# Kernel tuning notes

Hardware: AMD Instinct MI355X
Metric: run time of the kernel (lower is better)

## Reference

```python
import jax, jax.numpy as jnp
import numpy as np

EMBED = 1024
HEADS = 16
HEAD_DIM = EMBED // HEADS
SCALE = HEAD_DIM ** -0.5


def setup_inputs() -> dict:
    key = jax.random.key(0)
    ks = jax.random.split(key, 11)
    B, S, D = 2, 2048, EMBED
    s = D ** -0.5
    return {
        "Q": jax.random.normal(ks[0], (B, S, D), jnp.float32),
        "K": jax.random.normal(ks[1], (B, S, D), jnp.float32),
        "V": jax.random.normal(ks[2], (B, S, D), jnp.float32),
        "Wq": jax.random.normal(ks[3], (D, D), jnp.float32) * s,
        "bq": jax.random.normal(ks[4], (D,), jnp.float32) * 0.01,
        "Wk": jax.random.normal(ks[5], (D, D), jnp.float32) * s,
        "bk": jax.random.normal(ks[6], (D,), jnp.float32) * 0.01,
        "Wv": jax.random.normal(ks[7], (D, D), jnp.float32) * s,
        "bv": jax.random.normal(ks[8], (D,), jnp.float32) * 0.01,
        "Wo": jax.random.normal(ks[9], (D, D), jnp.float32) * s,
        "bo": jax.random.normal(ks[10], (D,), jnp.float32) * 0.01,
    }


def reference(Q, K, V, Wq, bq, Wk, bk, Wv, bv, Wo, bo):
    N, S, D = Q.shape
    H, Hd = HEADS, HEAD_DIM
    # linear projections (x @ W + b), then split heads: [N, S, H, Hd]
    q = (Q @ Wq + bq).reshape(N, S, H, Hd)
    k = (K @ Wk + bk).reshape(N, S, H, Hd)
    v = (V @ Wv + bv).reshape(N, S, H, Hd)
    # scaled dot-product attention, full [N,H,S,S] scores as in the original
    energy = jnp.einsum('nqhd,nkhd->nhqk', q, k) * SCALE
    attn = jax.nn.softmax(energy, axis=3)
    out = jnp.einsum('nhql,nlhd->nqhd', attn, v).reshape(N, S, D)
    return out @ Wo + bo
```

## Files before the change

### kernel.cpp

```cpp
#include <hip/hip_runtime.h>
#include <cstdint>


typedef _Float16 h8 __attribute__((ext_vector_type(8)));
typedef float f4 __attribute__((ext_vector_type(4)));
typedef float f16v __attribute__((ext_vector_type(16)));
typedef unsigned int u32x4 __attribute__((ext_vector_type(4)));
typedef const unsigned int __attribute__((address_space(1)))* gp1_t;
typedef unsigned int __attribute__((address_space(3)))* lp3_t;

#define FSWZ(r) ((((r) ^ ((r) >> 3))) & 7)

__device__ __forceinline__ void gld_lds16(const void* g, const void* l) {
  __builtin_amdgcn_global_load_lds((gp1_t)(uintptr_t)g,
                                   (lp3_t)(unsigned int)(uintptr_t)l, 16, 0, 0);
}
__device__ __forceinline__ unsigned pkh(float a, float b) {
  return __builtin_bit_cast(unsigned, __builtin_amdgcn_cvt_pkrtz(a, b));
}
__device__ __forceinline__ void plswap(unsigned& a, unsigned& b) {
  asm volatile("v_permlane32_swap_b32 %0, %1" : "+v"(a), "+v"(b));
}


__global__ void cvt_w4(const float* __restrict__ wq, const float* __restrict__ wk,
                       const float* __restrict__ wv, const float* __restrict__ wo,
                       _Float16* __restrict__ WT) {
  const int z = blockIdx.z;
  const float* W = (z == 0) ? wq : (z == 1) ? wk : (z == 2) ? wv : wo;
  _Float16* o = WT + (size_t)z * 1048576;
  const int k = blockIdx.x * 256 + threadIdx.x;
  const int n0 = blockIdx.y * 4;
  float4 w = *(const float4*)(W + (size_t)k * 1024 + n0);
  o[(size_t)(n0 + 0) * 1024 + k] = (_Float16)w.x;
  o[(size_t)(n0 + 1) * 1024 + k] = (_Float16)w.y;
  o[(size_t)(n0 + 2) * 1024 + k] = (_Float16)w.z;
  o[(size_t)(n0 + 3) * 1024 + k] = (_Float16)w.w;
}


#define A_LOAD(KT)                                                             \
  do {                                                                         \
    _Pragma("unroll") for (int i_ = 0; i_ < 4; ++i_) {                         \
      const int idx_ = i_ * 256 + tid;                                         \
      const int r_ = idx_ >> 3, g_ = idx_ & 7;                                 \
      const float* ap_ = A32 + (size_t)(row0 + r_) * 1024 + (KT) * 64 + g_ * 8;\
      fa[i_] = *(const float4*)ap_;                                            \
      fb[i_] = *(const float4*)(ap_ + 4);                                      \
    }                                                                          \
  } while (0)

#define A_WRITE(BUF)                                                           \
  do {                                                                         \
    _Pragma("unroll") for (int i_ = 0; i_ < 4; ++i_) {                         \
      const int idx_ = i_ * 256 + tid;                                         \
      const int r_ = idx_ >> 3, g_ = idx_ & 7;                                 \
      u32x4 w_ = {pkh(fa[i_].x, fa[i_].y), pkh(fa[i_].z, fa[i_].w),            \
                  pkh(fb[i_].x, fb[i_].y), pkh(fb[i_].z, fb[i_].w)};           \
      *(u32x4*)&As[BUF][r_ * 64 + ((g_ ^ FSWZ(r_)) << 3)] = w_;                \
    }                                                                          \
  } while (0)

#define B_STAGE(BUF, KT)                                                       \
  do {                                                                         \
    _Pragma("unroll") for (int rr_ = 0; rr_ < 4; ++rr_) {                      \
      const int idx_ = rr_ * 256 + tid;                                        \
      const int r_ = idx_ >> 3, g_ = idx_ & 7;                                 \
      gld_lds16(Bt + (size_t)(col0 + r_) * 1024 + (KT) * 64 + (g_ ^ FSWZ(r_)) * 8,\
                &Bs[BUF][(rr_ * 256 + wave * 64) * 8]);                        \
    }                                                                          \
  } while (0)

__global__ __launch_bounds__(256, 2) void gemm_qkv(const float* __restrict__ Qf,
                                                   const float* __restrict__ Kf,
                                                   const float* __restrict__ Vf,
                                                   const _Float16* __restrict__ WT,
                                                   const float* __restrict__ bq,
                                                   const float* __restrict__ bk,
                                                   const float* __restrict__ bv,
                                                   _Float16* __restrict__ qkv16) {
  __shared__ _Float16 As[2][8192];
  __shared__ _Float16 Bs[2][8192];
  const int z = blockIdx.z;
  const float* A32 = (z == 0) ? Qf : (z == 1) ? Kf : Vf;
  const _Float16* Bt = WT + (size_t)z * 1048576;
  const float* bias = (z == 0) ? bq : (z == 1) ? bk : bv;
  _Float16* out16 = qkv16 + (size_t)z * 4194304;
  const int tid = threadIdx.x;
  const int wave = tid >> 6, lane = tid & 63;
  const int lg = lane >> 4, ll = lane & 15;
  const int wr = wave >> 1, wc = wave & 1;
  const int row0 = blockIdx.x * 128, col0 = blockIdx.y * 128;
  f4 acc[4][4] = {};
  float4 fa[4], fb[4];
  A_LOAD(0);
  B_STAGE(0, 0);
  A_WRITE(0);
  __syncthreads();
  int cur = 0;
  for (int kt = 0; kt < 16; ++kt) {
    const bool pre = (kt + 1 < 16);
    if (pre) { A_LOAD(kt + 1); B_STAGE(cur ^ 1, kt + 1); }
#pragma unroll
    for (int kk = 0; kk < 2; ++kk) {
      h8 af[4], bf[4];
#pragma unroll
      for (int mi = 0; mi < 4; ++mi) {
        const int r = wr * 64 + mi * 16 + ll;
        af[mi] = *(const h8*)&As[cur][r * 64 + (((kk * 4 + lg) ^ FSWZ(r)) << 3)];
      }
#pragma unroll
      for (int ni = 0; ni < 4; ++ni) {
        const int r = wc * 64 + ni * 16 + ll;
        bf[ni] = *(const h8*)&Bs[cur][r * 64 + (((kk * 4 + lg) ^ FSWZ(r)) << 3)];
      }
#pragma unroll
      for (int mi = 0; mi < 4; ++mi)
#pragma unroll
        for (int ni = 0; ni < 4; ++ni)
          acc[mi][ni] = __builtin_amdgcn_mfma_f32_16x16x32_f16(af[mi], bf[ni],
                                                               acc[mi][ni], 0, 0, 0);
    }
    if (pre) A_WRITE(cur ^ 1);
    __syncthreads();
    cur ^= 1;
  }
#pragma unroll
  for (int ni = 0; ni < 4; ++ni) {
    const int c = col0 + wc * 64 + ni * 16 + ll;
    const float bv = bias[c];
#pragma unroll
    for (int mi = 0; mi < 4; ++mi) {
#pragma unroll
      for (int i = 0; i < 4; ++i) {
        const int r = row0 + wr * 64 + mi * 16 + lg * 4 + i;
        const float val = acc[mi][ni][i] + bv;
        const int b = r >> 11, s = r & 2047, h = c >> 6, hd = c & 63;
        out16[((size_t)((b * 16 + h) * 2048 + s)) * 64 + hd] = (_Float16)val;
      }
    }
  }
}


#define G_STAGE16(BUF, KT)                                                     \
  do {                                                                         \
    _Pragma("unroll") for (int rr_ = 0; rr_ < 4; ++rr_) {                      \
      const int idx_ = rr_ * 256 + tid;                                        \
      const int r_ = idx_ >> 3, g_ = idx_ & 7;                                 \
      const int lb_ = (rr_ * 256 + wave * 64) * 8;                             \
      gld_lds16(A16 + (size_t)(row0 + r_) * 1024 + (KT) * 64 + (g_ ^ FSWZ(r_)) * 8,\
                &As[BUF][lb_]);                                                \
      gld_lds16(WoT + (size_t)(col0 + r_) * 1024 + (KT) * 64 + (g_ ^ FSWZ(r_)) * 8,\
                &Bs[BUF][lb_]);                                                \
    }                                                                          \
  } while (0)

__global__ __launch_bounds__(256, 2) void gemm_out_k(const _Float16* __restrict__ A16,
                                                     const _Float16* __restrict__ WoT,
                                                     const float* __restrict__ bo,
                                                     float* __restrict__ out) {
  __shared__ _Float16 As[2][8192];
  __shared__ _Float16 Bs[2][8192];
  const int tid = threadIdx.x;
  const int wave = tid >> 6, lane = tid & 63;
  const int lg = lane >> 4, ll = lane & 15;
  const int wr = wave >> 1, wc = wave & 1;
  const int row0 = blockIdx.x * 128, col0 = blockIdx.y * 128;
  f4 acc[4][4] = {};
  G_STAGE16(0, 0);
  __syncthreads();
  int cur = 0;
  for (int kt = 0; kt < 16; ++kt) {
    if (kt + 1 < 16) G_STAGE16(cur ^ 1, kt + 1);
#pragma unroll
    for (int kk = 0; kk < 2; ++kk) {
      h8 af[4], bf[4];
#pragma unroll
      for (int mi = 0; mi < 4; ++mi) {
        const int r = wr * 64 + mi * 16 + ll;
        af[mi] = *(const h8*)&As[cur][r * 64 + (((kk * 4 + lg) ^ FSWZ(r)) << 3)];
      }
#pragma unroll
      for (int ni = 0; ni < 4; ++ni) {
        const int r = wc * 64 + ni * 16 + ll;
        bf[ni] = *(const h8*)&Bs[cur][r * 64 + (((kk * 4 + lg) ^ FSWZ(r)) << 3)];
      }
#pragma unroll
      for (int mi = 0; mi < 4; ++mi)
#pragma unroll
        for (int ni = 0; ni < 4; ++ni)
          acc[mi][ni] = __builtin_amdgcn_mfma_f32_16x16x32_f16(af[mi], bf[ni],
                                                               acc[mi][ni], 0, 0, 0);
    }
    __syncthreads();
    cur ^= 1;
  }
#pragma unroll
  for (int ni = 0; ni < 4; ++ni) {
    const int c = col0 + wc * 64 + ni * 16 + ll;
    const float bv = bo[c];
#pragma unroll
    for (int mi = 0; mi < 4; ++mi)
#pragma unroll
      for (int i = 0; i < 4; ++i) {
        const int r = row0 + wr * 64 + mi * 16 + lg * 4 + i;
        out[(size_t)r * 1024 + c] = acc[mi][ni][i] + bv;
      }
  }
}


#define STAGE_K(BUF, KT)                                                      \
  do {                                                                        \
    _Pragma("unroll") for (int rr_ = 0; rr_ < 2; ++rr_) {                     \
      const int idx_ = rr_ * 256 + tid;                                       \
      const int r_ = idx_ >> 3, g_ = idx_ & 7;                                \
      gld_lds16(kbp + (size_t)((KT) * 64 + r_) * 64 + ((g_ ^ FSWZ(r_)) * 8),  \
                &Ks[BUF][(rr_ * 256 + wave * 64) * 8]);                       \
    }                                                                         \
  } while (0)

#define LOAD_V(KT, VA, VC)                                                    \
  do {                                                                        \
    const _Float16* vp_ = vbp + (size_t)((KT) * 64 + vkey0) * 64 + vhd0;      \
    VA = *(const uint4*)vp_;                                                  \
    VC = *(const uint4*)(vp_ + 64);                                           \
  } while (0)

#define WRITE_V(BUF, VA, VC)                                                  \
  do {                                                                        \
    const unsigned short* pa_ = (const unsigned short*)&VA;                   \
    const unsigned short* pc_ = (const unsigned short*)&VC;                   \
    _Pragma("unroll") for (int j_ = 0; j_ < 8; ++j_) {                        \
      const int row_ = vhd0 + j_;                                             \
      *(unsigned*)&Vt[BUF][row_ * 64 + (((vkey0 >> 3) ^ FSWZ(row_)) << 3) +   \
                           (vkey0 & 7)] =                                     \
          (unsigned)pa_[j_] | ((unsigned)pc_[j_] << 16);                      \
    }                                                                         \
  } while (0)

#define PV_STEP(SX, PP, KBP)                                                  \
  do {                                                                        \
    unsigned wA = pkh(SX[(PP) + 0], SX[(PP) + 1]);                            \
    unsigned wB = pkh(SX[(PP) + 2], SX[(PP) + 3]);                            \
    unsigned wC = pkh(SX[(PP) + 4], SX[(PP) + 5]);                            \
    unsigned wD = pkh(SX[(PP) + 6], SX[(PP) + 7]);                            \
    plswap(wA, wC);                                                           \
    plswap(wB, wD);                                                           \
    u32x4 afu = {wA, wB, wC, wD};                                             \
    h8 af = __builtin_bit_cast(h8, afu);                                      \
    const int c_ = (KBP) * 2 + hi;                                            \
    h8 vf0 = *(const h8*)&Vt[cur][l31 * 64 + ((c_ ^ FSWZ(l31)) << 3)];        \
    h8 vf1 = *(const h8*)&Vt[cur][(32 + l31) * 64 +                           \
                                  ((c_ ^ FSWZ(32 + l31)) << 3)];              \
    acc0 = __builtin_amdgcn_mfma_f32_32x32x16_f16(af, vf0, acc0, 0, 0, 0);    \
    acc1 = __builtin_amdgcn_mfma_f32_32x32x16_f16(af, vf1, acc1, 0, 0, 0);    \
  } while (0)

__global__ __launch_bounds__(256, 4) void attn_kernel(
    const _Float16* __restrict__ q16, const _Float16* __restrict__ k16,
    const _Float16* __restrict__ v16, _Float16* __restrict__ Op,
    float2* __restrict__ mlp) {
  __shared__ _Float16 Ks[2][4096];
  __shared__ _Float16 Vt[2][4096];
  __shared__ float Fb[4][32];
  const int tid = threadIdx.x;
  const int wave = tid >> 6, lane = tid & 63;
  const int l31 = lane & 31, hi = lane >> 5;
  const int blk = blockIdx.x;
  const int xcd = blk & 7, j = blk >> 3;
  const int bh = xcd * 4 + (j >> 5);
  const int split = (j >> 4) & 1;
  const int qb = j & 15;
  const int q0w = qb * 128 + wave * 32;
  const _Float16* qbp = q16 + (size_t)bh * 131072;
  const _Float16* kbp = k16 + (size_t)bh * 131072 + (size_t)split * 65536;
  const _Float16* vbp = v16 + (size_t)bh * 131072 + (size_t)split * 65536;
  const int vkey0 = (tid & 31) * 2, vhd0 = (tid >> 5) * 8;

  h8 qf0 = *(const h8*)(qbp + (size_t)(q0w + l31) * 64 + 0 + hi * 8);
  h8 qf1 = *(const h8*)(qbp + (size_t)(q0w + l31) * 64 + 16 + hi * 8);
  h8 qf2 = *(const h8*)(qbp + (size_t)(q0w + l31) * 64 + 32 + hi * 8);
  h8 qf3 = *(const h8*)(qbp + (size_t)(q0w + l31) * 64 + 48 + hi * 8);

  f16v acc0 = {}, acc1 = {};
  float mval = -1e30f, lsum = 0.f;
  const float C = 0.125f * 1.44269504089f;

  uint4 va, vc;
  STAGE_K(0, 0);
  LOAD_V(0, va, vc);
  WRITE_V(0, va, vc);
  __syncthreads();

  int cur = 0;
  for (int kt = 0; kt < 16; ++kt) {
    const bool pre = (kt + 1 < 16);
    if (pre) { STAGE_K(cur ^ 1, kt + 1); LOAD_V(kt + 1, va, vc); }

    f16v s0 = {}, s1 = {};
    __builtin_amdgcn_s_setprio(1);
#pragma unroll
    for (int kc = 0; kc < 4; ++kc) {
      const int c = kc * 2 + hi;
      h8 k0 = *(const h8*)&Ks[cur][l31 * 64 + ((c ^ FSWZ(l31)) << 3)];
      h8 k1 = *(const h8*)&Ks[cur][(32 + l31) * 64 + ((c ^ FSWZ(32 + l31)) << 3)];
      h8 qf = (kc == 0) ? qf0 : (kc == 1) ? qf1 : (kc == 2) ? qf2 : qf3;
      s0 = __builtin_amdgcn_mfma_f32_32x32x16_f16(k0, qf, s0, 0, 0, 0);
      s1 = __builtin_amdgcn_mfma_f32_32x32x16_f16(k1, qf, s1, 0, 0, 0);
    }
    __builtin_amdgcn_s_setprio(0);

    float t[8];
#pragma unroll
    for (int j2 = 0; j2 < 8; ++j2)
      t[j2] = fmaxf(fmaxf(s0[j2], s0[j2 + 8]), fmaxf(s1[j2], s1[j2 + 8]));
    float pm = fmaxf(fmaxf(fmaxf(t[0], t[1]), fmaxf(t[2], t[3])),
                     fmaxf(fmaxf(t[4], t[5]), fmaxf(t[6], t[7])));
    pm = fmaxf(pm, __shfl_xor(pm, 32));
    const float pms = pm * C;

    if (__any(pms > mval + 8.0f)) {
      const float mnew = fmaxf(mval, pms);
      const float f = __builtin_amdgcn_exp2f(mval - mnew);
      mval = mnew;
      lsum *= f;
      Fb[wave][l31] = f;
      const f4 fr0 = *(const f4*)&Fb[wave][0 + 4 * hi];
      const f4 fr1 = *(const f4*)&Fb[wave][8 + 4 * hi];
      const f4 fr2 = *(const f4*)&Fb[wave][16 + 4 * hi];
      const f4 fr3 = *(const f4*)&Fb[wave][24 + 4 * hi];
#pragma unroll
      for (int r = 0; r < 16; ++r) {
        const float fx = (r < 4 ? fr0 : r < 8 ? fr1 : r < 12 ? fr2 : fr3)[r & 3];
        acc0[r] *= fx;
        acc1[r] *= fx;
      }
    }

#pragma unroll
    for (int r = 0; r < 16; ++r) {
      s0[r] = __builtin_amdgcn_exp2f(s0[r] * C - mval);
      s1[r] = __builtin_amdgcn_exp2f(s1[r] * C - mval);
    }
    float z[8];
#pragma unroll
    for (int j2 = 0; j2 < 8; ++j2)
      z[j2] = (s0[j2] + s0[j2 + 8]) + (s1[j2] + s1[j2 + 8]);
    lsum += ((z[0] + z[1]) + (z[2] + z[3])) + ((z[4] + z[5]) + (z[6] + z[7]));

    __builtin_amdgcn_s_setprio(1);
    PV_STEP(s0, 0, 0);
    PV_STEP(s0, 8, 1);
    PV_STEP(s1, 0, 2);
    PV_STEP(s1, 8, 3);
    __builtin_amdgcn_s_setprio(0);

    if (pre) WRITE_V(cur ^ 1, va, vc);
    __syncthreads();
    cur ^= 1;
  }

  lsum += __shfl_xor(lsum, 32);
  if (!hi) mlp[split * 65536 + bh * 2048 + q0w + l31] = make_float2(mval, lsum);
  const float inv = 1.0f / lsum;
  Fb[wave][l31] = inv;
  const f4 ir0 = *(const f4*)&Fb[wave][0 + 4 * hi];
  const f4 ir1 = *(const f4*)&Fb[wave][8 + 4 * hi];
  const f4 ir2 = *(const f4*)&Fb[wave][16 + 4 * hi];
  const f4 ir3 = *(const f4*)&Fb[wave][24 + 4 * hi];
#pragma unroll
  for (int r = 0; r < 16; ++r) {
    const float fx = (r < 4 ? ir0 : r < 8 ? ir1 : r < 12 ? ir2 : ir3)[r & 3];
    const int srow = q0w + (r & 3) + 8 * (r >> 2) + 4 * hi;
    _Float16* op = Op + (size_t)split * 4194304 +
                   ((size_t)(bh * 2048 + srow)) * 64 + l31;
    op[0] = (_Float16)(acc0[r] * fx);
    op[32] = (_Float16)(acc1[r] * fx);
  }
}


__global__ __launch_bounds__(256) void cmb(const _Float16* __restrict__ Op,
                                           const float2* __restrict__ mlp,
                                           _Float16* __restrict__ ao) {
  const int gid = blockIdx.x * 256 + threadIdx.x;
  const int R = gid >> 3, o = gid & 7;
  const float2 a = mlp[R];
  const float2 c = mlp[65536 + R];
  const float M = fmaxf(a.x, c.x);
  float w0 = __builtin_amdgcn_exp2f(a.x - M) * a.y;
  float w1 = __builtin_amdgcn_exp2f(c.x - M) * c.y;
  const float inv = 1.0f / (w0 + w1);
  w0 *= inv;
  w1 *= inv;
  h8 p0 = *(const h8*)(Op + (size_t)R * 64 + o * 8);
  h8 p1 = *(const h8*)(Op + 4194304 + (size_t)R * 64 + o * 8);
  const int bh = R >> 11, s = R & 2047, b = bh >> 4, h = bh & 15;
  h8 r;
#pragma unroll
  for (int j = 0; j < 8; ++j)
    r[j] = (_Float16)(w0 * (float)p0[j] + w1 * (float)p1[j]);
  *(h8*)(ao + ((size_t)(b * 2048 + s)) * 1024 + h * 64 + o * 8) = r;
}


extern "C" void kernel_launch(void* const* d_in, const int* in_sizes, int n_in,
                              void* d_out, int out_size, void* d_ws, size_t ws_size,
                              hipStream_t stream) {
  const float* Q  = (const float*)d_in[0];
  const float* K  = (const float*)d_in[1];
  const float* V  = (const float*)d_in[2];
  const float* Wq = (const float*)d_in[3];
  const float* bq = (const float*)d_in[4];
  const float* Wk = (const float*)d_in[5];
  const float* bk = (const float*)d_in[6];
  const float* Wv = (const float*)d_in[7];
  const float* bv = (const float*)d_in[8];
  const float* Wo = (const float*)d_in[9];
  const float* bo = (const float*)d_in[10];

  _Float16* H      = (_Float16*)d_ws;
  _Float16* Op     = H;
  float2*   mlp    = (float2*)(H + 8388608);
  _Float16* WT     = H + 12582912;
  _Float16* qkv16  = H + 16777216;
  _Float16* aout16 = H + 29360128;
  float* out = (float*)d_out;

  cvt_w4<<<dim3(4, 256, 4), 256, 0, stream>>>(Wq, Wk, Wv, Wo, WT);
  gemm_qkv<<<dim3(32, 8, 3), 256, 0, stream>>>(Q, K, V, WT, bq, bk, bv, qkv16);
  attn_kernel<<<dim3(1024), 256, 0, stream>>>(qkv16, qkv16 + 4194304,
                                              qkv16 + 8388608, Op, mlp);
  cmb<<<dim3(2048), 256, 0, stream>>>(Op, mlp, aout16);
  gemm_out_k<<<dim3(32, 8), 256, 0, stream>>>(aout16, WT + 3145728, bo, out);
}
```

Before: 135.5 us.

## Drop split-K attention, software-pipeline QK/PV, fold softmax scale into Q projection

The attention kernel no longer splits keys in two, and the combine kernel is removed. Each block now walks all 32 key tiles and writes the normalized output directly in [B,S,D] layout. The loop is software-pipelined so the QK MFMA for the next tile overlaps the PV MFMA for the current one, with the softmax and packing done between barriers. The softmax scale times log2(e) is folded into the Q projection epilogue, which saves a multiply per score. The output GEMM tile narrows to 128x64 so it launches twice as many blocks, and attention occupancy bounds drop to 2 waves per SIMD.

```diff
diff --git a/kernel.cpp b/kernel.cpp
--- a/kernel.cpp
+++ b/kernel.cpp
@@ -86,6 +86,7 @@
   const _Float16* Bt = WT + (size_t)z * 1048576;
   const float* bias = (z == 0) ? bq : (z == 1) ? bk : bv;
   _Float16* out16 = qkv16 + (size_t)z * 4194304;
+  const float scl = (z == 0) ? 0.18033688f : 1.0f;
   const int tid = threadIdx.x;
   const int wave = tid >> 6, lane = tid & 63;
   const int lg = lane >> 4, ll = lane & 15;
@@ -134,7 +135,7 @@
 #pragma unroll
       for (int i = 0; i < 4; ++i) {
         const int r = row0 + wr * 64 + mi * 16 + lg * 4 + i;
-        const float val = acc[mi][ni][i] + bv;
+        const float val = (acc[mi][ni][i] + bv) * scl;
         const int b = r >> 11, s = r & 2047, h = c >> 6, hd = c & 63;
         out16[((size_t)((b * 16 + h) * 2048 + s)) * 64 + hd] = (_Float16)val;
       }
@@ -143,16 +144,19 @@
 }
 
 
-#define G_STAGE16(BUF, KT)                                                     \
+#define GO_STAGE(BUF, KT)                                                      \
   do {                                                                         \
     _Pragma("unroll") for (int rr_ = 0; rr_ < 4; ++rr_) {                      \
       const int idx_ = rr_ * 256 + tid;                                        \
       const int r_ = idx_ >> 3, g_ = idx_ & 7;                                 \
-      const int lb_ = (rr_ * 256 + wave * 64) * 8;                             \
       gld_lds16(A16 + (size_t)(row0 + r_) * 1024 + (KT) * 64 + (g_ ^ FSWZ(r_)) * 8,\
-                &As[BUF][lb_]);                                                \
+                &As[BUF][(rr_ * 256 + wave * 64) * 8]);                        \
+    }                                                                          \
+    _Pragma("unroll") for (int rr_ = 0; rr_ < 2; ++rr_) {                      \
+      const int idx_ = rr_ * 256 + tid;                                        \
+      const int r_ = idx_ >> 3, g_ = idx_ & 7;                                 \
       gld_lds16(WoT + (size_t)(col0 + r_) * 1024 + (KT) * 64 + (g_ ^ FSWZ(r_)) * 8,\
-                &Bs[BUF][lb_]);                                                \
+                &Bs[BUF][(rr_ * 256 + wave * 64) * 8]);                        \
     }                                                                          \
   } while (0)
 
@@ -161,35 +165,35 @@
                                                      const float* __restrict__ bo,
                                                      float* __restrict__ out) {
   __shared__ _Float16 As[2][8192];
-  __shared__ _Float16 Bs[2][8192];
+  __shared__ _Float16 Bs[2][4096];
   const int tid = threadIdx.x;
   const int wave = tid >> 6, lane = tid & 63;
   const int lg = lane >> 4, ll = lane & 15;
   const int wr = wave >> 1, wc = wave & 1;
-  const int row0 = blockIdx.x * 128, col0 = blockIdx.y * 128;
-  f4 acc[4][4] = {};
-  G_STAGE16(0, 0);
+  const int row0 = blockIdx.x * 128, col0 = blockIdx.y * 64;
+  f4 acc[4][2] = {};
+  GO_STAGE(0, 0);
   __syncthreads();
   int cur = 0;
   for (int kt = 0; kt < 16; ++kt) {
-    if (kt + 1 < 16) G_STAGE16(cur ^ 1, kt + 1);
+    if (kt + 1 < 16) GO_STAGE(cur ^ 1, kt + 1);
 #pragma unroll
     for (int kk = 0; kk < 2; ++kk) {
-      h8 af[4], bf[4];
+      h8 af[4], bf[2];
 #pragma unroll
       for (int mi = 0; mi < 4; ++mi) {
         const int r = wr * 64 + mi * 16 + ll;
         af[mi] = *(const h8*)&As[cur][r * 64 + (((kk * 4 + lg) ^ FSWZ(r)) << 3)];
       }
 #pragma unroll
-      for (int ni = 0; ni < 4; ++ni) {
-        const int r = wc * 64 + ni * 16 + ll;
+      for (int ni = 0; ni < 2; ++ni) {
+        const int r = wc * 32 + ni * 16 + ll;
         bf[ni] = *(const h8*)&Bs[cur][r * 64 + (((kk * 4 + lg) ^ FSWZ(r)) << 3)];
       }
 #pragma unroll
       for (int mi = 0; mi < 4; ++mi)
 #pragma unroll
-        for (int ni = 0; ni < 4; ++ni)
+        for (int ni = 0; ni < 2; ++ni)
           acc[mi][ni] = __builtin_amdgcn_mfma_f32_16x16x32_f16(af[mi], bf[ni],
                                                                acc[mi][ni], 0, 0, 0);
     }
@@ -197,8 +201,8 @@
     cur ^= 1;
   }
 #pragma unroll
-  for (int ni = 0; ni < 4; ++ni) {
-    const int c = col0 + wc * 64 + ni * 16 + ll;
+  for (int ni = 0; ni < 2; ++ni) {
+    const int c = col0 + wc * 32 + ni * 16 + ll;
     const float bv = bo[c];
 #pragma unroll
     for (int mi = 0; mi < 4; ++mi)
@@ -221,17 +225,17 @@
     }                                                                         \
   } while (0)
 
-#define LOAD_V(KT, VA, VC)                                                    \
+#define LOAD_V(KT)                                                            \
   do {                                                                        \
     const _Float16* vp_ = vbp + (size_t)((KT) * 64 + vkey0) * 64 + vhd0;      \
-    VA = *(const uint4*)vp_;                                                  \
-    VC = *(const uint4*)(vp_ + 64);                                           \
-  } while (0)
-
-#define WRITE_V(BUF, VA, VC)                                                  \
-  do {                                                                        \
-    const unsigned short* pa_ = (const unsigned short*)&VA;                   \
-    const unsigned short* pc_ = (const unsigned short*)&VC;                   \
+    va = *(const uint4*)vp_;                                                  \
+    vc = *(const uint4*)(vp_ + 64);                                           \
+  } while (0)
+
+#define WRITE_V(BUF)                                                          \
+  do {                                                                        \
+    const unsigned short* pa_ = (const unsigned short*)&va;                   \
+    const unsigned short* pc_ = (const unsigned short*)&vc;                   \
     _Pragma("unroll") for (int j_ = 0; j_ < 8; ++j_) {                        \
       const int row_ = vhd0 + j_;                                             \
       *(unsigned*)&Vt[BUF][row_ * 64 + (((vkey0 >> 3) ^ FSWZ(row_)) << 3) +   \
@@ -240,7 +244,22 @@
     }                                                                         \
   } while (0)
 
-#define PV_STEP(SX, PP, KBP)                                                  \
+#define QK_COMPUTE(BUF, S0, S1)                                               \
+  do {                                                                        \
+    S0 = (f16v){};                                                            \
+    S1 = (f16v){};                                                            \
+    _Pragma("unroll") for (int kc_ = 0; kc_ < 4; ++kc_) {                     \
+      const int c_ = kc_ * 2 + hi;                                            \
+      h8 k0_ = *(const h8*)&Ks[BUF][l31 * 64 + ((c_ ^ FSWZ(l31)) << 3)];      \
+      h8 k1_ = *(const h8*)&Ks[BUF][(32 + l31) * 64 +                         \
+                                    ((c_ ^ FSWZ(32 + l31)) << 3)];            \
+      h8 qf_ = (kc_ == 0) ? qf0 : (kc_ == 1) ? qf1 : (kc_ == 2) ? qf2 : qf3;  \
+      S0 = __builtin_amdgcn_mfma_f32_32x32x16_f16(k0_, qf_, S0, 0, 0, 0);     \
+      S1 = __builtin_amdgcn_mfma_f32_32x32x16_f16(k1_, qf_, S1, 0, 0, 0);     \
+    }                                                                         \
+  } while (0)
+
+#define PACK_AF(DST, SX, PP)                                                  \
   do {                                                                        \
     unsigned wA = pkh(SX[(PP) + 0], SX[(PP) + 1]);                            \
     unsigned wB = pkh(SX[(PP) + 2], SX[(PP) + 3]);                            \
@@ -248,20 +267,66 @@
     unsigned wD = pkh(SX[(PP) + 6], SX[(PP) + 7]);                            \
     plswap(wA, wC);                                                           \
     plswap(wB, wD);                                                           \
-    u32x4 afu = {wA, wB, wC, wD};                                             \
-    h8 af = __builtin_bit_cast(h8, afu);                                      \
-    const int c_ = (KBP) * 2 + hi;                                            \
-    h8 vf0 = *(const h8*)&Vt[cur][l31 * 64 + ((c_ ^ FSWZ(l31)) << 3)];        \
-    h8 vf1 = *(const h8*)&Vt[cur][(32 + l31) * 64 +                           \
-                                  ((c_ ^ FSWZ(32 + l31)) << 3)];              \
-    acc0 = __builtin_amdgcn_mfma_f32_32x32x16_f16(af, vf0, acc0, 0, 0, 0);    \
-    acc1 = __builtin_amdgcn_mfma_f32_32x32x16_f16(af, vf1, acc1, 0, 0, 0);    \
-  } while (0)
-
-__global__ __launch_bounds__(256, 4) void attn_kernel(
+    DST = (u32x4){wA, wB, wC, wD};                                            \
+  } while (0)
+
+#define SM_PK(S0, S1)                                                         \
+  do {                                                                        \
+    float t_[8];                                                              \
+    _Pragma("unroll") for (int j2_ = 0; j2_ < 8; ++j2_)                       \
+        t_[j2_] = fmaxf(fmaxf(S0[j2_], S0[j2_ + 8]),                          \
+                        fmaxf(S1[j2_], S1[j2_ + 8]));                         \
+    float pm_ = fmaxf(fmaxf(fmaxf(t_[0], t_[1]), fmaxf(t_[2], t_[3])),        \
+                      fmaxf(fmaxf(t_[4], t_[5]), fmaxf(t_[6], t_[7])));       \
+    pm_ = fmaxf(pm_, __shfl_xor(pm_, 32));                                    \
+    if (__any(pm_ > mval + 8.0f)) {                                           \
+      const float mn_ = fmaxf(mval, pm_);                                     \
+      const float f_ = __builtin_amdgcn_exp2f(mval - mn_);                    \
+      mval = mn_;                                                             \
+      lsum *= f_;                                                             \
+      Fb[wave][l31] = f_;                                                     \
+      const f4 fr0_ = *(const f4*)&Fb[wave][0 + 4 * hi];                      \
+      const f4 fr1_ = *(const f4*)&Fb[wave][8 + 4 * hi];                      \
+      const f4 fr2_ = *(const f4*)&Fb[wave][16 + 4 * hi];                     \
+      const f4 fr3_ = *(const f4*)&Fb[wave][24 + 4 * hi];                     \
+      _Pragma("unroll") for (int r_ = 0; r_ < 16; ++r_) {                     \
+        const float fx_ =                                                     \
+            (r_ < 4 ? fr0_ : r_ < 8 ? fr1_ : r_ < 12 ? fr2_ : fr3_)[r_ & 3];  \
+        acc0[r_] *= fx_;                                                      \
+        acc1[r_] *= fx_;                                                      \
+      }                                                                       \
+    }                                                                         \
+    _Pragma("unroll") for (int r_ = 0; r_ < 16; ++r_) {                       \
+      S0[r_] = __builtin_amdgcn_exp2f(S0[r_] - mval);                         \
+      S1[r_] = __builtin_amdgcn_exp2f(S1[r_] - mval);                         \
+    }                                                                         \
+    float z_[8];                                                              \
+    _Pragma("unroll") for (int j2_ = 0; j2_ < 8; ++j2_)                       \
+        z_[j2_] = (S0[j2_] + S0[j2_ + 8]) + (S1[j2_] + S1[j2_ + 8]);          \
+    lsum += ((z_[0] + z_[1]) + (z_[2] + z_[3])) +                             \
+            ((z_[4] + z_[5]) + (z_[6] + z_[7]));                              \
+    PACK_AF(afr[0], S0, 0);                                                   \
+    PACK_AF(afr[1], S0, 8);                                                   \
+    PACK_AF(afr[2], S1, 0);                                                   \
+    PACK_AF(afr[3], S1, 8);                                                   \
+  } while (0)
+
+#define PV_APPLY(BUF)                                                         \
+  do {                                                                        \
+    _Pragma("unroll") for (int i_ = 0; i_ < 4; ++i_) {                        \
+      const int c_ = i_ * 2 + hi;                                             \
+      h8 vf0_ = *(const h8*)&Vt[BUF][l31 * 64 + ((c_ ^ FSWZ(l31)) << 3)];     \
+      h8 vf1_ = *(const h8*)&Vt[BUF][(32 + l31) * 64 +                        \
+                                     ((c_ ^ FSWZ(32 + l31)) << 3)];           \
+      h8 af_ = __builtin_bit_cast(h8, afr[i_]);                               \
+      acc0 = __builtin_amdgcn_mfma_f32_32x32x16_f16(af_, vf0_, acc0, 0, 0, 0);\
+      acc1 = __builtin_amdgcn_mfma_f32_32x32x16_f16(af_, vf1_, acc1, 0, 0, 0);\
+    }                                                                         \
+  } while (0)
+
+__global__ __launch_bounds__(256, 2) void attn_kernel(
     const _Float16* __restrict__ q16, const _Float16* __restrict__ k16,
-    const _Float16* __restrict__ v16, _Float16* __restrict__ Op,
-    float2* __restrict__ mlp) {
+    const _Float16* __restrict__ v16, _Float16* __restrict__ aout) {
   __shared__ _Float16 Ks[2][4096];
   __shared__ _Float16 Vt[2][4096];
   __shared__ float Fb[4][32];
@@ -270,13 +335,12 @@
   const int l31 = lane & 31, hi = lane >> 5;
   const int blk = blockIdx.x;
   const int xcd = blk & 7, j = blk >> 3;
-  const int bh = xcd * 4 + (j >> 5);
-  const int split = (j >> 4) & 1;
+  const int bh = xcd * 4 + (j >> 4);
   const int qb = j & 15;
   const int q0w = qb * 128 + wave * 32;
   const _Float16* qbp = q16 + (size_t)bh * 131072;
-  const _Float16* kbp = k16 + (size_t)bh * 131072 + (size_t)split * 65536;
-  const _Float16* vbp = v16 + (size_t)bh * 131072 + (size_t)split * 65536;
+  const _Float16* kbp = k16 + (size_t)bh * 131072;
+  const _Float16* vbp = v16 + (size_t)bh * 131072;
   const int vkey0 = (tid & 31) * 2, vhd0 = (tid >> 5) * 8;
 
   h8 qf0 = *(const h8*)(qbp + (size_t)(q0w + l31) * 64 + 0 + hi * 8);
@@ -285,124 +349,53 @@
   h8 qf3 = *(const h8*)(qbp + (size_t)(q0w + l31) * 64 + 48 + hi * 8);
 
   f16v acc0 = {}, acc1 = {};
+  f16v sr0 = {}, sr1 = {};
+  u32x4 afr[4];
   float mval = -1e30f, lsum = 0.f;
-  const float C = 0.125f * 1.44269504089f;
-
   uint4 va, vc;
+
   STAGE_K(0, 0);
-  LOAD_V(0, va, vc);
-  WRITE_V(0, va, vc);
+  LOAD_V(0);
+  WRITE_V(0);
   __syncthreads();
-
-  int cur = 0;
-  for (int kt = 0; kt < 16; ++kt) {
-    const bool pre = (kt + 1 < 16);
-    if (pre) { STAGE_K(cur ^ 1, kt + 1); LOAD_V(kt + 1, va, vc); }
-
-    f16v s0 = {}, s1 = {};
+  QK_COMPUTE(0, sr0, sr1);
+  STAGE_K(1, 1);
+  LOAD_V(1);
+  WRITE_V(1);
+  SM_PK(sr0, sr1);
+  __syncthreads();
+
+  for (int t = 0; t < 31; ++t) {
+    const int A = t & 1, B = A ^ 1;
+    if (t + 2 < 32) LOAD_V(t + 2);
     __builtin_amdgcn_s_setprio(1);
-#pragma unroll
-    for (int kc = 0; kc < 4; ++kc) {
-      const int c = kc * 2 + hi;
-      h8 k0 = *(const h8*)&Ks[cur][l31 * 64 + ((c ^ FSWZ(l31)) << 3)];
-      h8 k1 = *(const h8*)&Ks[cur][(32 + l31) * 64 + ((c ^ FSWZ(32 + l31)) << 3)];
-      h8 qf = (kc == 0) ? qf0 : (kc == 1) ? qf1 : (kc == 2) ? qf2 : qf3;
-      s0 = __builtin_amdgcn_mfma_f32_32x32x16_f16(k0, qf, s0, 0, 0, 0);
-      s1 = __builtin_amdgcn_mfma_f32_32x32x16_f16(k1, qf, s1, 0, 0, 0);
-    }
+    QK_COMPUTE(B, sr0, sr1);
+    PV_APPLY(A);
     __builtin_amdgcn_s_setprio(0);
-
-    float t[8];
-#pragma unroll
-    for (int j2 = 0; j2 < 8; ++j2)
-      t[j2] = fmaxf(fmaxf(s0[j2], s0[j2 + 8]), fmaxf(s1[j2], s1[j2 + 8]));
-    float pm = fmaxf(fmaxf(fmaxf(t[0], t[1]), fmaxf(t[2], t[3])),
-                     fmaxf(fmaxf(t[4], t[5]), fmaxf(t[6], t[7])));
-    pm = fmaxf(pm, __shfl_xor(pm, 32));
-    const float pms = pm * C;
-
-    if (__any(pms > mval + 8.0f)) {
-      const float mnew = fmaxf(mval, pms);
-      const float f = __builtin_amdgcn_exp2f(mval - mnew);
-      mval = mnew;
-      lsum *= f;
-      Fb[wave][l31] = f;
-      const f4 fr0 = *(const f4*)&Fb[wave][0 + 4 * hi];
-      const f4 fr1 = *(const f4*)&Fb[wave][8 + 4 * hi];
-      const f4 fr2 = *(const f4*)&Fb[wave][16 + 4 * hi];
-      const f4 fr3 = *(const f4*)&Fb[wave][24 + 4 * hi];
-#pragma unroll
-      for (int r = 0; r < 16; ++r) {
-        const float fx = (r < 4 ? fr0 : r < 8 ? fr1 : r < 12 ? fr2 : fr3)[r & 3];
-        acc0[r] *= fx;
-        acc1[r] *= fx;
-      }
-    }
-
-#pragma unroll
-    for (int r = 0; r < 16; ++r) {
-      s0[r] = __builtin_amdgcn_exp2f(s0[r] * C - mval);
-      s1[r] = __builtin_amdgcn_exp2f(s1[r] * C - mval);
-    }
-    float z[8];
-#pragma unroll
-    for (int j2 = 0; j2 < 8; ++j2)
-      z[j2] = (s0[j2] + s0[j2 + 8]) + (s1[j2] + s1[j2 + 8]);
-    lsum += ((z[0] + z[1]) + (z[2] + z[3])) + ((z[4] + z[5]) + (z[6] + z[7]));
-
-    __builtin_amdgcn_s_setprio(1);
-    PV_STEP(s0, 0, 0);
-    PV_STEP(s0, 8, 1);
-    PV_STEP(s1, 0, 2);
-    PV_STEP(s1, 8, 3);
-    __builtin_amdgcn_s_setprio(0);
-
-    if (pre) WRITE_V(cur ^ 1, va, vc);
+    __builtin_amdgcn_sched_barrier(0);
     __syncthreads();
-    cur ^= 1;
-  }
+    if (t + 2 < 32) { STAGE_K(A, t + 2); WRITE_V(A); }
+    SM_PK(sr0, sr1);
+    __syncthreads();
+  }
+  PV_APPLY(1);
 
   lsum += __shfl_xor(lsum, 32);
-  if (!hi) mlp[split * 65536 + bh * 2048 + q0w + l31] = make_float2(mval, lsum);
   const float inv = 1.0f / lsum;
   Fb[wave][l31] = inv;
   const f4 ir0 = *(const f4*)&Fb[wave][0 + 4 * hi];
   const f4 ir1 = *(const f4*)&Fb[wave][8 + 4 * hi];
   const f4 ir2 = *(const f4*)&Fb[wave][16 + 4 * hi];
   const f4 ir3 = *(const f4*)&Fb[wave][24 + 4 * hi];
+  const int b = bh >> 4, h = bh & 15;
 #pragma unroll
   for (int r = 0; r < 16; ++r) {
     const float fx = (r < 4 ? ir0 : r < 8 ? ir1 : r < 12 ? ir2 : ir3)[r & 3];
     const int srow = q0w + (r & 3) + 8 * (r >> 2) + 4 * hi;
-    _Float16* op = Op + (size_t)split * 4194304 +
-                   ((size_t)(bh * 2048 + srow)) * 64 + l31;
+    _Float16* op = aout + ((size_t)(b * 2048 + srow)) * 1024 + h * 64 + l31;
     op[0] = (_Float16)(acc0[r] * fx);
     op[32] = (_Float16)(acc1[r] * fx);
   }
-}
-
-
-__global__ __launch_bounds__(256) void cmb(const _Float16* __restrict__ Op,
-                                           const float2* __restrict__ mlp,
-                                           _Float16* __restrict__ ao) {
-  const int gid = blockIdx.x * 256 + threadIdx.x;
-  const int R = gid >> 3, o = gid & 7;
-  const float2 a = mlp[R];
-  const float2 c = mlp[65536 + R];
-  const float M = fmaxf(a.x, c.x);
-  float w0 = __builtin_amdgcn_exp2f(a.x - M) * a.y;
-  float w1 = __builtin_amdgcn_exp2f(c.x - M) * c.y;
-  const float inv = 1.0f / (w0 + w1);
-  w0 *= inv;
-  w1 *= inv;
-  h8 p0 = *(const h8*)(Op + (size_t)R * 64 + o * 8);
-  h8 p1 = *(const h8*)(Op + 4194304 + (size_t)R * 64 + o * 8);
-  const int bh = R >> 11, s = R & 2047, b = bh >> 4, h = bh & 15;
-  h8 r;
-#pragma unroll
-  for (int j = 0; j < 8; ++j)
-    r[j] = (_Float16)(w0 * (float)p0[j] + w1 * (float)p1[j]);
-  *(h8*)(ao + ((size_t)(b * 2048 + s)) * 1024 + h * 64 + o * 8) = r;
 }
 
 
@@ -422,8 +415,6 @@
   const float* bo = (const float*)d_in[10];
 
   _Float16* H      = (_Float16*)d_ws;
-  _Float16* Op     = H;
-  float2*   mlp    = (float2*)(H + 8388608);
   _Float16* WT     = H + 12582912;
   _Float16* qkv16  = H + 16777216;
   _Float16* aout16 = H + 29360128;
@@ -431,8 +422,7 @@
 
   cvt_w4<<<dim3(4, 256, 4), 256, 0, stream>>>(Wq, Wk, Wv, Wo, WT);
   gemm_qkv<<<dim3(32, 8, 3), 256, 0, stream>>>(Q, K, V, WT, bq, bk, bv, qkv16);
-  attn_kernel<<<dim3(1024), 256, 0, stream>>>(qkv16, qkv16 + 4194304,
-                                              qkv16 + 8388608, Op, mlp);
-  cmb<<<dim3(2048), 256, 0, stream>>>(Op, mlp, aout16);
-  gemm_out_k<<<dim3(32, 8), 256, 0, stream>>>(aout16, WT + 3145728, bo, out);
-}
+  attn_kernel<<<dim3(512), 256, 0, stream>>>(qkv16, qkv16 + 4194304,
+                                             qkv16 + 8388608, aout16);
+  gemm_out_k<<<dim3(32, 16), 256, 0, stream>>>(aout16, WT + 3145728, bo, out);
+}
```

After: 125.0 us. -7.8%, faster.
